# Kernel optimization log

Hardware: AMD Instinct MI355X
Metric: run time of the kernel (lower is better)

Reference implementation:

```python
import jax, jax.numpy as jnp
import numpy as np

B, S, D = 4, 2048, 512
K = 8192  # codebook_size
COMMIT_W = 0.25
ENT_W = 0.1
ENT_TEMP = 0.01
EPS = 1e-8


def setup_inputs() -> dict:
    key = jax.random.key(0)
    kx, kc = jax.random.split(key)
    x = jax.random.normal(kx, (B, S, D), dtype=jnp.float32)
    # variance_scaling(1.0, 'fan_in', 'uniform'): bound = sqrt(3 / fan_in)
    bound = np.sqrt(3.0 / D)
    codebook = jax.random.uniform(kc, (K, D), dtype=jnp.float32, minval=-bound, maxval=bound)
    return {"x": x, "codebook": codebook}


def _entropy_loss(affinity, temperature, eps=EPS):
    # affinity: (B, S, K) -> flatten tokens
    flat = affinity.reshape((-1, affinity.shape[-1])) / temperature
    probs = jax.nn.softmax(flat, axis=-1)
    log_probs = jax.nn.log_softmax(flat + eps, axis=-1)
    avg_probs = jnp.mean(probs, axis=0)
    avg_entropy = -jnp.sum(avg_probs * jnp.log(avg_probs + eps))
    sample_entropy = -jnp.mean(jnp.sum(probs * log_probs, axis=-1))
    return sample_entropy - avg_entropy


def reference(x, codebook):
    # the original cdist, without the (B,S,K,D) intermediate).
    x_sq = jnp.sum(x * x, axis=-1, keepdims=True)          # (B,S,1)
    c_sq = jnp.sum(codebook * codebook, axis=-1)           # (K,)
    dots = jnp.einsum('bsd,kd->bsk', x, codebook)          # (B,S,K)
    distances = jnp.sqrt(jnp.maximum(x_sq - 2.0 * dots + c_sq, 0.0))
    indices = jnp.argmin(distances, axis=-1)               # (B,S)
    # one_hot @ codebook == gather
    quantized = jnp.take(codebook, indices, axis=0)        # (B,S,D)

    sg = jax.lax.stop_gradient
    # optax.l2_loss(p, t) = 0.5 * (p - t)^2
    commit_loss = 0.5 * jnp.mean((x - sg(quantized)) ** 2) * COMMIT_W
    codebook_loss = 0.5 * jnp.mean((sg(x) - quantized) ** 2)
    entropy_loss = _entropy_loss(-distances, ENT_TEMP) * ENT_W
    loss = codebook_loss + commit_loss + entropy_loss

    quantized_st = x + sg(quantized - x)  # straight-through estimator
    return (quantized_st, loss, commit_loss, codebook_loss, entropy_loss, indices)
```

## Files before the change

### kernel.cpp

```cpp
#include <hip/hip_runtime.h>
#include <math.h>

#define NTOK 8192
#define KCODES 8192
#define DDIM 512
#define QELEMS (NTOK * DDIM)

#define NCHUNK 8
#define CPC (KCODES / NCHUNK)
#define LDK 40

constexpr size_t S_PART  = 0;
constexpr size_t S_XSQ   = 524288;
constexpr size_t S_CSQ   = S_XSQ + NTOK;
constexpr size_t S_LSE   = S_CSQ + KCODES;
constexpr size_t S_PLOGP = S_LSE + NTOK;
constexpr size_t S_D2    = S_PLOGP + NTOK;
constexpr size_t S_AVG   = S_D2 + NTOK;
constexpr size_t S_I1    = S_AVG + KCODES;
constexpr size_t S_I2    = S_I1 + NTOK;

#define NCHUNK_F 16
#define CPC_F (KCODES / NCHUNK_F)

constexpr size_t FS_PART  = 0;
constexpr size_t FS_XSQ   = 1048576;
constexpr size_t FS_CSQ   = FS_XSQ + NTOK;
constexpr size_t FS_LSE   = FS_CSQ + KCODES;
constexpr size_t FS_PLOGP = FS_LSE + NTOK;
constexpr size_t FS_D2    = FS_PLOGP + NTOK;
constexpr size_t FS_AVG   = FS_D2 + NTOK;
constexpr size_t FS_I1    = FS_AVG + KCODES;
constexpr size_t FS_I2    = FS_I1 + NTOK;

constexpr size_t WS_NEED_BYTES = 4ull * (size_t)QELEMS * 2ull;

typedef __attribute__((ext_vector_type(8))) short bf16x8;
typedef __attribute__((ext_vector_type(4))) float f32x4;

__device__ __forceinline__ bool better(float v, int i, float v2, int i2) {
  return v > v2 || (v == v2 && i < i2);
}

__device__ __forceinline__ void cvt_hilo(float f, unsigned& h, unsigned& l) {
  const unsigned u = __float_as_uint(f);
  h = u >> 16;
  const float lf = f - __uint_as_float(u & 0xFFFF0000u);
  l = __float_as_uint(lf) >> 16;
}

__device__ __forceinline__ void gll16(const unsigned short* g, const short* l) {
  __builtin_amdgcn_global_load_lds(
      (const __attribute__((address_space(1))) unsigned int*)g,
      (__attribute__((address_space(3))) unsigned int*)l, 16, 0, 0);
}

__global__ __launch_bounds__(64) void sq_kernel(const float* __restrict__ x,
                                                const float* __restrict__ cb,
                                                float* __restrict__ dout,
                                                size_t offXsq, size_t offCsq) {
  const int row = blockIdx.x;
  const int lane = threadIdx.x;
  const float* src = (row < KCODES) ? (cb + (size_t)row * DDIM)
                                    : (x + (size_t)(row - KCODES) * DDIM);
  float4 v0 = reinterpret_cast<const float4*>(src)[lane];
  float4 v1 = reinterpret_cast<const float4*>(src)[lane + 64];
  float s = v0.x*v0.x + v0.y*v0.y + v0.z*v0.z + v0.w*v0.w
          + v1.x*v1.x + v1.y*v1.y + v1.z*v1.z + v1.w*v1.w;
  #pragma unroll
  for (int o = 32; o; o >>= 1) s += __shfl_down(s, o);
  if (lane == 0) {
    if (row < KCODES) dout[offCsq + row] = s;
    else              dout[offXsq + (row - KCODES)] = s;
  }
}

__global__ void zero_kernel(float* __restrict__ dout, size_t offAvg) {
  dout[offAvg + blockIdx.x * 256 + threadIdx.x] = 0.f;
}

__global__ __launch_bounds__(256) void cvt_kernel(const float* __restrict__ x,
                                                  const float* __restrict__ cb,
                                                  unsigned short* __restrict__ ws) {
  const size_t fid = (size_t)blockIdx.x * 256 + threadIdx.x;
  const size_t half = (size_t)QELEMS / 4;
  const bool isX = fid < half;
  const float* src = isX ? x : cb;
  unsigned short* dh = ws + (isX ? 0 : (size_t)2 * QELEMS);
  unsigned short* dl = dh + QELEMS;
  const size_t f = isX ? fid : fid - half;
  const size_t e0 = f * 4;
  const int row = (int)(e0 >> 9);
  const int k = (int)(e0 & 511);
  const int tile = row >> 7, r = row & 127;
  const int kt = k >> 5, gg = (k >> 3) & 3, e = k & 7;
  const float4 v = *reinterpret_cast<const float4*>(src + e0);
  unsigned h0, h1, h2, h3, l0, l1, l2, l3;
  cvt_hilo(v.x, h0, l0); cvt_hilo(v.y, h1, l1);
  cvt_hilo(v.z, h2, l2); cvt_hilo(v.w, h3, l3);
  uint2 hp, lp;
  hp.x = h0 | (h1 << 16); hp.y = h2 | (h3 << 16);
  lp.x = l0 | (l1 << 16); lp.y = l2 | (l3 << 16);
  const size_t dst = (((size_t)tile * 16 + kt) * 4 + gg) * 1024 + (size_t)r * 8 + e;
  *reinterpret_cast<uint2*>(dh + dst) = hp;
  *reinterpret_cast<uint2*>(dl + dst) = lp;
}


#define MFMA_KSTEP_F                                                          \
  {                                                                           \
    bf16x8 a_h[4], a_l[4];                                                    \
    _Pragma("unroll")                                                         \
    for (int fi = 0; fi < 4; ++fi) {                                          \
      const int ra = (wr * 64 + fi * 16 + lx) * 8 + kg * 1024;                \
      a_h[fi] = *reinterpret_cast<const bf16x8*>(&lds4[0][ra]);               \
      a_l[fi] = *reinterpret_cast<const bf16x8*>(&lds4[1][ra]);               \
    }                                                                         \
    _Pragma("unroll")                                                         \
    for (int fj = 0; fj < 4; ++fj) {                                          \
      const int rb = (wc * 64 + fj * 16 + lx) * 8 + kg * 1024;                \
      const bf16x8 b_h = *reinterpret_cast<const bf16x8*>(&lds4[2][rb]);      \
      const bf16x8 b_l = *reinterpret_cast<const bf16x8*>(&lds4[3][rb]);      \
      _Pragma("unroll")                                                       \
      for (int fi = 0; fi < 4; ++fi) {                                        \
        acc[fi][fj] = __builtin_amdgcn_mfma_f32_16x16x32_bf16(a_h[fi], b_h, acc[fi][fj], 0, 0, 0); \
        acc[fi][fj] = __builtin_amdgcn_mfma_f32_16x16x32_bf16(a_l[fi], b_h, acc[fi][fj], 0, 0, 0); \
        acc[fi][fj] = __builtin_amdgcn_mfma_f32_16x16x32_bf16(a_h[fi], b_l, acc[fi][fj], 0, 0, 0); \
      }                                                                       \
    }                                                                         \
  }

#define STAGE_F(kt_)                                                          \
  {                                                                           \
    const unsigned short* p = gb + (((size_t)tile * 16 + (kt_)) * 4096) + l * 8; \
    const short* lb = &lds4[w][0];                                            \
    _Pragma("unroll")                                                         \
    for (int s8 = 0; s8 < 8; ++s8) gll16(p + s8 * 512, lb + s8 * 512);        \
  }

__global__ __launch_bounds__(256, 3) void pass1f(const unsigned short* __restrict__ ws,
                                                 float* __restrict__ dout) {
  __shared__ short lds4[4][4096];
  __shared__ float stats[2][128][6];
  const int tid = threadIdx.x;
  const int l = tid & 63;
  const int w = tid >> 6;
  const int wr = w >> 1, wc = w & 1;
  const int kg = l >> 4, lx = l & 15;
  const int m0 = blockIdx.y * 128;
  const int atile = blockIdx.y;
  const int chunk = blockIdx.x;

  if (tid < 128) {
    #pragma unroll
    for (int q = 0; q < 2; ++q) {
      stats[q][tid][0] = -1e30f; stats[q][tid][1] = 0.f; stats[q][tid][2] = 0.f;
      stats[q][tid][3] = -1e30f;
      stats[q][tid][4] = __int_as_float(0x7fffffff);
      stats[q][tid][5] = __int_as_float(0x7fffffff);
    }
  }

  float xs[16];
  #pragma unroll
  for (int fi = 0; fi < 4; ++fi)
    #pragma unroll
    for (int v = 0; v < 4; ++v)
      xs[fi * 4 + v] = dout[FS_XSQ + m0 + wr * 64 + fi * 16 + kg * 4 + v];

  const unsigned short* gb = ws + (size_t)w * (size_t)QELEMS;

  for (int st = 0; st < CPC_F / 128; ++st) {
    const int n0 = chunk * CPC_F + st * 128;
    const int tile = (w < 2) ? atile : (n0 >> 7);
    f32x4 acc[4][4];
    #pragma unroll
    for (int fi = 0; fi < 4; ++fi)
      #pragma unroll
      for (int fj = 0; fj < 4; ++fj)
        acc[fi][fj] = (f32x4){0.f, 0.f, 0.f, 0.f};

    for (int kt = 0; kt < DDIM / 32; ++kt) {
      __syncthreads();
      STAGE_F(kt);
      __syncthreads();
      MFMA_KSTEP_F;
    }

    const int colbase = n0 + wc * 64 + lx;
    float cs[4];
    #pragma unroll
    for (int fj = 0; fj < 4; ++fj) cs[fj] = dout[FS_CSQ + colbase + fj * 16];

    #pragma unroll
    for (int fi = 0; fi < 4; ++fi) {
      #pragma unroll
      for (int v = 0; v < 4; ++v) {
        const float xsv = xs[fi * 4 + v];
        float fv[4];
        #pragma unroll
        for (int fj = 0; fj < 4; ++fj) {
          const float d2 = fmaxf(fmaf(-2.f, acc[fi][fj][v], xsv) + cs[fj], 0.f);
          fv[fj] = -100.f * sqrtf(d2);
        }
        float v1 = fv[0], v2 = -1e30f;
        int i1 = colbase, i2 = 0x7fffffff;
        #pragma unroll
        for (int fj = 1; fj < 4; ++fj) {
          const int c = colbase + fj * 16;
          if (better(fv[fj], c, v1, i1)) { v2 = v1; i2 = i1; v1 = fv[fj]; i1 = c; }
          else if (better(fv[fj], c, v2, i2)) { v2 = fv[fj]; i2 = c; }
        }
        #pragma unroll
        for (int mask = 1; mask < 16; mask <<= 1) {
          const float ov1 = __shfl_xor(v1, mask);
          const float ov2 = __shfl_xor(v2, mask);
          const int oi1 = __shfl_xor(i1, mask);
          const int oi2 = __shfl_xor(i2, mask);
          float n1, n2; int ni1, ni2;
          if (better(ov1, oi1, v1, i1)) {
            n1 = ov1; ni1 = oi1;
            if (better(v1, i1, ov2, oi2)) { n2 = v1; ni2 = i1; } else { n2 = ov2; ni2 = oi2; }
          } else {
            n1 = v1; ni1 = i1;
            if (better(ov1, oi1, v2, i2)) { n2 = ov1; ni2 = oi1; } else { n2 = v2; ni2 = i2; }
          }
          v1 = n1; i1 = ni1; v2 = n2; i2 = ni2;
        }
        float z = 0.f, s = 0.f;
        #pragma unroll
        for (int fj = 0; fj < 4; ++fj) {
          const float ge = fv[fj] - v1;
          const float e = __expf(ge);
          z += e; s = fmaf(e, ge, s);
        }
        #pragma unroll
        for (int mask = 1; mask < 16; mask <<= 1) {
          z += __shfl_xor(z, mask);
          s += __shfl_xor(s, mask);
        }
        if (lx == 0) {
          const int r = wr * 64 + fi * 16 + kg * 4 + v;
          float* st_ = &stats[wc][r][0];
          const float ov1 = st_[0], oz = st_[1], os = st_[2], ov2 = st_[3];
          const int oi1 = __float_as_int(st_[4]), oi2 = __float_as_int(st_[5]);
          const float M = fmaxf(v1, ov1);
          const float ea = __expf(v1 - M), eb = __expf(ov1 - M);
          st_[1] = ea * z + eb * oz;
          st_[2] = ea * (s + (v1 - M) * z) + eb * (os + (ov1 - M) * oz);
          float n1, n2; int ni1, ni2;
          if (better(ov1, oi1, v1, i1)) {
            n1 = ov1; ni1 = oi1;
            if (better(v1, i1, ov2, oi2)) { n2 = v1; ni2 = i1; } else { n2 = ov2; ni2 = oi2; }
          } else {
            n1 = v1; ni1 = i1;
            if (better(ov1, oi1, v2, i2)) { n2 = ov1; ni2 = oi1; } else { n2 = v2; ni2 = i2; }
          }
          st_[0] = n1; st_[3] = n2;
          st_[4] = __int_as_float(ni1);
          st_[5] = __int_as_float(ni2);
        }
      }
    }
  }

  __syncthreads();
  if (tid < 128) {
    float v1 = stats[0][tid][0], z = stats[0][tid][1], s = stats[0][tid][2], v2 = stats[0][tid][3];
    int i1 = __float_as_int(stats[0][tid][4]), i2 = __float_as_int(stats[0][tid][5]);
    const float ov1 = stats[1][tid][0], oz = stats[1][tid][1];
    const float os = stats[1][tid][2], ov2 = stats[1][tid][3];
    const int oi1 = __float_as_int(stats[1][tid][4]), oi2 = __float_as_int(stats[1][tid][5]);
    const float M = fmaxf(v1, ov1);
    const float ea = __expf(v1 - M), eb = __expf(ov1 - M);
    const float nz = ea * z + eb * oz;
    const float ns = ea * (s + (v1 - M) * z) + eb * (os + (ov1 - M) * oz);
    float n1, n2; int ni1, ni2;
    if (better(ov1, oi1, v1, i1)) {
      n1 = ov1; ni1 = oi1;
      if (better(v1, i1, ov2, oi2)) { n2 = v1; ni2 = i1; } else { n2 = ov2; ni2 = oi2; }
    } else {
      n1 = v1; ni1 = i1;
      if (better(ov1, oi1, v2, i2)) { n2 = ov1; ni2 = oi1; } else { n2 = v2; ni2 = i2; }
    }
    float* p = dout + FS_PART + ((size_t)(m0 + tid) * NCHUNK_F + chunk) * 8;
    p[0] = n1; p[1] = nz; p[2] = ns; p[3] = n2;
    p[4] = __int_as_float(ni1); p[5] = __int_as_float(ni2);
  }
}

__global__ __launch_bounds__(256, 3) void colf(const unsigned short* __restrict__ ws,
                                               float* __restrict__ dout) {
  __shared__ short lds4[4][4096];
  __shared__ float red[4][64];
  const int tid = threadIdx.x;
  const int l = tid & 63;
  const int w = tid >> 6;
  const int wr = w >> 1, wc = w & 1;
  const int kg = l >> 4, lx = l & 15;
  const int m0 = blockIdx.y * 128;
  const int atile = blockIdx.y;
  const int chunk = blockIdx.x;

  float xs[16], lse[16];
  #pragma unroll
  for (int fi = 0; fi < 4; ++fi)
    #pragma unroll
    for (int v = 0; v < 4; ++v) {
      const int r = m0 + wr * 64 + fi * 16 + kg * 4 + v;
      xs[fi * 4 + v] = dout[FS_XSQ + r];
      lse[fi * 4 + v] = dout[FS_LSE + r];
    }

  const unsigned short* gb = ws + (size_t)w * (size_t)QELEMS;

  for (int st = 0; st < CPC_F / 128; ++st) {
    const int n0 = chunk * CPC_F + st * 128;
    const int tile = (w < 2) ? atile : (n0 >> 7);
    f32x4 acc[4][4];
    #pragma unroll
    for (int fi = 0; fi < 4; ++fi)
      #pragma unroll
      for (int fj = 0; fj < 4; ++fj)
        acc[fi][fj] = (f32x4){0.f, 0.f, 0.f, 0.f};

    for (int kt = 0; kt < DDIM / 32; ++kt) {
      __syncthreads();
      STAGE_F(kt);
      __syncthreads();
      MFMA_KSTEP_F;
    }

    const int colbase = n0 + wc * 64 + lx;
    float cs[4];
    #pragma unroll
    for (int fj = 0; fj < 4; ++fj) cs[fj] = dout[FS_CSQ + colbase + fj * 16];

    float colsum[4] = {0.f, 0.f, 0.f, 0.f};
    #pragma unroll
    for (int fi = 0; fi < 4; ++fi) {
      #pragma unroll
      for (int v = 0; v < 4; ++v) {
        const float xsv = xs[fi * 4 + v];
        const float lsev = lse[fi * 4 + v];
        #pragma unroll
        for (int fj = 0; fj < 4; ++fj) {
          const float d2 = fmaxf(fmaf(-2.f, acc[fi][fj][v], xsv) + cs[fj], 0.f);
          const float f = -100.f * sqrtf(d2);
          colsum[fj] += __expf(f - lsev);
        }
      }
    }
    #pragma unroll
    for (int fj = 0; fj < 4; ++fj) {
      colsum[fj] += __shfl_xor(colsum[fj], 16);
      colsum[fj] += __shfl_xor(colsum[fj], 32);
    }
    __syncthreads();
    if (kg == 0) {
      #pragma unroll
      for (int fj = 0; fj < 4; ++fj) red[w][fj * 16 + lx] = colsum[fj];
    }
    __syncthreads();
    if (tid < 128) {
      const int wcc = tid >> 6, c = tid & 63;
      atomicAdd(&dout[FS_AVG + n0 + tid], red[wcc][c] + red[wcc + 2][c]);
    }
  }
}


#define STAGE_TILES(kt_)                                                      \
  {                                                                           \
    const int kb = (kt_) * 32 + sc;                                           \
    _Pragma("unroll")                                                         \
    for (int rep = 0; rep < 4; ++rep) {                                       \
      const int row = sr + rep * 32;                                          \
      const float4 av = *reinterpret_cast<const float4*>(                     \
          x + (size_t)(m0 + row) * DDIM + kb);                                \
      const float4 bv = *reinterpret_cast<const float4*>(                     \
          cb + (size_t)(n0 + row) * DDIM + kb);                               \
      unsigned h0, h1, h2, h3, l0, l1, l2, l3;                                \
      uint2 t;                                                                \
      cvt_hilo(av.x, h0, l0); cvt_hilo(av.y, h1, l1);                         \
      cvt_hilo(av.z, h2, l2); cvt_hilo(av.w, h3, l3);                         \
      t.x = h0 | (h1 << 16); t.y = h2 | (h3 << 16);                           \
      *reinterpret_cast<uint2*>(&Ah[row][sc]) = t;                            \
      t.x = l0 | (l1 << 16); t.y = l2 | (l3 << 16);                           \
      *reinterpret_cast<uint2*>(&Al[row][sc]) = t;                            \
      cvt_hilo(bv.x, h0, l0); cvt_hilo(bv.y, h1, l1);                         \
      cvt_hilo(bv.z, h2, l2); cvt_hilo(bv.w, h3, l3);                         \
      t.x = h0 | (h1 << 16); t.y = h2 | (h3 << 16);                           \
      *reinterpret_cast<uint2*>(&Bh[row][sc]) = t;                            \
      t.x = l0 | (l1 << 16); t.y = l2 | (l3 << 16);                           \
      *reinterpret_cast<uint2*>(&Bl[row][sc]) = t;                            \
    }                                                                         \
  }

#define MFMA_KSTEP                                                            \
  {                                                                           \
    bf16x8 a_h[4], a_l[4];                                                    \
    _Pragma("unroll")                                                         \
    for (int fi = 0; fi < 4; ++fi) {                                          \
      a_h[fi] = *reinterpret_cast<const bf16x8*>(&Ah[ar + fi * 16][koff]);    \
      a_l[fi] = *reinterpret_cast<const bf16x8*>(&Al[ar + fi * 16][koff]);    \
    }                                                                         \
    _Pragma("unroll")                                                         \
    for (int fj = 0; fj < 4; ++fj) {                                          \
      const bf16x8 b_h = *reinterpret_cast<const bf16x8*>(&Bh[br + fj * 16][koff]); \
      const bf16x8 b_l = *reinterpret_cast<const bf16x8*>(&Bl[br + fj * 16][koff]); \
      _Pragma("unroll")                                                       \
      for (int fi = 0; fi < 4; ++fi) {                                        \
        acc[fi][fj] = __builtin_amdgcn_mfma_f32_16x16x32_bf16(a_h[fi], b_h, acc[fi][fj], 0, 0, 0); \
        acc[fi][fj] = __builtin_amdgcn_mfma_f32_16x16x32_bf16(a_l[fi], b_h, acc[fi][fj], 0, 0, 0); \
        acc[fi][fj] = __builtin_amdgcn_mfma_f32_16x16x32_bf16(a_h[fi], b_l, acc[fi][fj], 0, 0, 0); \
      }                                                                       \
    }                                                                         \
  }

__global__ __launch_bounds__(256) void pass1_mfma(const float* __restrict__ x,
                                                  const float* __restrict__ cb,
                                                  float* __restrict__ dout) {
  __shared__ short Ah[128][LDK], Al[128][LDK], Bh[128][LDK], Bl[128][LDK];
  __shared__ float stats[2][128][6];
  const int tid = threadIdx.x;
  const int l = tid & 63;
  const int w = tid >> 6;
  const int wr = w >> 1, wc = w & 1;
  const int g = l >> 4, lx = l & 15;
  const int ar = wr * 64 + lx;
  const int br = wc * 64 + lx;
  const int koff = g * 8;
  const int sr = tid >> 3;
  const int sc = (tid & 7) * 4;
  const int m0 = blockIdx.y * 128;
  const int chunk = blockIdx.x;

  if (tid < 128) {
    #pragma unroll
    for (int q = 0; q < 2; ++q) {
      stats[q][tid][0] = -1e30f; stats[q][tid][1] = 0.f; stats[q][tid][2] = 0.f;
      stats[q][tid][3] = -1e30f;
      stats[q][tid][4] = __int_as_float(0x7fffffff);
      stats[q][tid][5] = __int_as_float(0x7fffffff);
    }
  }

  float xs[16];
  #pragma unroll
  for (int fi = 0; fi < 4; ++fi)
    #pragma unroll
    for (int v = 0; v < 4; ++v)
      xs[fi * 4 + v] = dout[S_XSQ + m0 + wr * 64 + fi * 16 + g * 4 + v];

  for (int st = 0; st < CPC / 128; ++st) {
    const int n0 = chunk * CPC + st * 128;
    f32x4 acc[4][4];
    #pragma unroll
    for (int fi = 0; fi < 4; ++fi)
      #pragma unroll
      for (int fj = 0; fj < 4; ++fj)
        acc[fi][fj] = (f32x4){0.f, 0.f, 0.f, 0.f};

    for (int kt = 0; kt < DDIM / 32; ++kt) {
      __syncthreads();
      STAGE_TILES(kt);
      __syncthreads();
      MFMA_KSTEP;
    }

    const int colbase = n0 + wc * 64 + lx;
    float cs[4];
    #pragma unroll
    for (int fj = 0; fj < 4; ++fj) cs[fj] = dout[S_CSQ + colbase + fj * 16];

    #pragma unroll
    for (int fi = 0; fi < 4; ++fi) {
      #pragma unroll
      for (int v = 0; v < 4; ++v) {
        const float xsv = xs[fi * 4 + v];
        float fv[4];
        #pragma unroll
        for (int fj = 0; fj < 4; ++fj) {
          const float d2 = fmaxf(fmaf(-2.f, acc[fi][fj][v], xsv) + cs[fj], 0.f);
          fv[fj] = -100.f * sqrtf(d2);
        }
        float v1 = fv[0], v2 = -1e30f;
        int i1 = colbase, i2 = 0x7fffffff;
        #pragma unroll
        for (int fj = 1; fj < 4; ++fj) {
          const int c = colbase + fj * 16;
          if (better(fv[fj], c, v1, i1)) { v2 = v1; i2 = i1; v1 = fv[fj]; i1 = c; }
          else if (better(fv[fj], c, v2, i2)) { v2 = fv[fj]; i2 = c; }
        }
        #pragma unroll
        for (int mask = 1; mask < 16; mask <<= 1) {
          const float ov1 = __shfl_xor(v1, mask);
          const float ov2 = __shfl_xor(v2, mask);
          const int oi1 = __shfl_xor(i1, mask);
          const int oi2 = __shfl_xor(i2, mask);
          float n1, n2; int ni1, ni2;
          if (better(ov1, oi1, v1, i1)) {
            n1 = ov1; ni1 = oi1;
            if (better(v1, i1, ov2, oi2)) { n2 = v1; ni2 = i1; } else { n2 = ov2; ni2 = oi2; }
          } else {
            n1 = v1; ni1 = i1;
            if (better(ov1, oi1, v2, i2)) { n2 = ov1; ni2 = oi1; } else { n2 = v2; ni2 = i2; }
          }
          v1 = n1; i1 = ni1; v2 = n2; i2 = ni2;
        }
        float z = 0.f, s = 0.f;
        #pragma unroll
        for (int fj = 0; fj < 4; ++fj) {
          const float ge = fv[fj] - v1;
          const float e = __expf(ge);
          z += e; s = fmaf(e, ge, s);
        }
        #pragma unroll
        for (int mask = 1; mask < 16; mask <<= 1) {
          z += __shfl_xor(z, mask);
// ... 274 lines not shown
```

Before: 663.5 us.

## Double-buffer LDS staging and keep per-row online softmax stats in registers

Both the row-statistics and column-sum GEMM kernels now double-buffer their LDS tiles. The next k-slice is loaded asynchronously while MFMAs run on the current one, and each step needs one barrier instead of two. In pass1f the per-row argmin, top-2 and online softmax statistics are kept per lane in registers across all column tiles and reduced by shuffles only once at the end, instead of after every tile. In exchange, LDS use doubles and register pressure rises, so the occupancy hint is lowered from 3 to 2 blocks per CU.

```diff
diff --git a/kernel.cpp b/kernel.cpp
--- a/kernel.cpp
+++ b/kernel.cpp
@@ -107,20 +107,31 @@
 }
 
 
-#define MFMA_KSTEP_F                                                          \
+#define STAGE2(b_, s_)                                                        \
   {                                                                           \
+    const int st_ = (s_) >> 4, kt_ = (s_) & 15;                               \
+    const int tile_ = (w < 2) ? atile : ((chunk * CPC_F + st_ * 128) >> 7);   \
+    const unsigned short* p = gb + (((size_t)tile_ * 16 + kt_) * 4096) + l * 8; \
+    const short* lb = &lds4[b_][w][0];                                        \
+    _Pragma("unroll")                                                         \
+    for (int s8 = 0; s8 < 8; ++s8) gll16(p + s8 * 512, lb + s8 * 512);        \
+  }
+
+#define MFMA_KSTEP2(b_)                                                       \
+  {                                                                           \
+    const short* Lb = &lds4[b_][0][0];                                        \
     bf16x8 a_h[4], a_l[4];                                                    \
     _Pragma("unroll")                                                         \
     for (int fi = 0; fi < 4; ++fi) {                                          \
       const int ra = (wr * 64 + fi * 16 + lx) * 8 + kg * 1024;                \
-      a_h[fi] = *reinterpret_cast<const bf16x8*>(&lds4[0][ra]);               \
-      a_l[fi] = *reinterpret_cast<const bf16x8*>(&lds4[1][ra]);               \
+      a_h[fi] = *reinterpret_cast<const bf16x8*>(Lb + ra);                    \
+      a_l[fi] = *reinterpret_cast<const bf16x8*>(Lb + 4096 + ra);             \
     }                                                                         \
     _Pragma("unroll")                                                         \
     for (int fj = 0; fj < 4; ++fj) {                                          \
       const int rb = (wc * 64 + fj * 16 + lx) * 8 + kg * 1024;                \
-      const bf16x8 b_h = *reinterpret_cast<const bf16x8*>(&lds4[2][rb]);      \
-      const bf16x8 b_l = *reinterpret_cast<const bf16x8*>(&lds4[3][rb]);      \
+      const bf16x8 b_h = *reinterpret_cast<const bf16x8*>(Lb + 8192 + rb);    \
+      const bf16x8 b_l = *reinterpret_cast<const bf16x8*>(Lb + 12288 + rb);   \
       _Pragma("unroll")                                                       \
       for (int fi = 0; fi < 4; ++fi) {                                        \
         acc[fi][fj] = __builtin_amdgcn_mfma_f32_16x16x32_bf16(a_h[fi], b_h, acc[fi][fj], 0, 0, 0); \
@@ -130,17 +141,9 @@
     }                                                                         \
   }
 
-#define STAGE_F(kt_)                                                          \
-  {                                                                           \
-    const unsigned short* p = gb + (((size_t)tile * 16 + (kt_)) * 4096) + l * 8; \
-    const short* lb = &lds4[w][0];                                            \
-    _Pragma("unroll")                                                         \
-    for (int s8 = 0; s8 < 8; ++s8) gll16(p + s8 * 512, lb + s8 * 512);        \
-  }
-
-__global__ __launch_bounds__(256, 3) void pass1f(const unsigned short* __restrict__ ws,
+__global__ __launch_bounds__(256, 2) void pass1f(const unsigned short* __restrict__ ws,
                                                  float* __restrict__ dout) {
-  __shared__ short lds4[4][4096];
+  __shared__ short lds4[2][4][4096];
   __shared__ float stats[2][128][6];
   const int tid = threadIdx.x;
   const int l = tid & 63;
@@ -151,16 +154,6 @@
   const int atile = blockIdx.y;
   const int chunk = blockIdx.x;
 
-  if (tid < 128) {
-    #pragma unroll
-    for (int q = 0; q < 2; ++q) {
-      stats[q][tid][0] = -1e30f; stats[q][tid][1] = 0.f; stats[q][tid][2] = 0.f;
-      stats[q][tid][3] = -1e30f;
-      stats[q][tid][4] = __int_as_float(0x7fffffff);
-      stats[q][tid][5] = __int_as_float(0x7fffffff);
-    }
-  }
-
   float xs[16];
   #pragma unroll
   for (int fi = 0; fi < 4; ++fi)
@@ -168,99 +161,106 @@
     for (int v = 0; v < 4; ++v)
       xs[fi * 4 + v] = dout[FS_XSQ + m0 + wr * 64 + fi * 16 + kg * 4 + v];
 
+  float rv1[16], rv2[16], rz[16], rs[16];
+  int ri1[16], ri2[16];
+  #pragma unroll
+  for (int r = 0; r < 16; ++r) {
+    rv1[r] = -1e30f; rv2[r] = -1e30f; rz[r] = 0.f; rs[r] = 0.f;
+    ri1[r] = 0x7fffffff; ri2[r] = 0x7fffffff;
+  }
+
   const unsigned short* gb = ws + (size_t)w * (size_t)QELEMS;
 
-  for (int st = 0; st < CPC_F / 128; ++st) {
-    const int n0 = chunk * CPC_F + st * 128;
-    const int tile = (w < 2) ? atile : (n0 >> 7);
-    f32x4 acc[4][4];
-    #pragma unroll
-    for (int fi = 0; fi < 4; ++fi)
-      #pragma unroll
-      for (int fj = 0; fj < 4; ++fj)
-        acc[fi][fj] = (f32x4){0.f, 0.f, 0.f, 0.f};
-
-    for (int kt = 0; kt < DDIM / 32; ++kt) {
-      __syncthreads();
-      STAGE_F(kt);
-      __syncthreads();
-      MFMA_KSTEP_F;
-    }
-
-    const int colbase = n0 + wc * 64 + lx;
-    float cs[4];
-    #pragma unroll
-    for (int fj = 0; fj < 4; ++fj) cs[fj] = dout[FS_CSQ + colbase + fj * 16];
-
-    #pragma unroll
-    for (int fi = 0; fi < 4; ++fi) {
-      #pragma unroll
-      for (int v = 0; v < 4; ++v) {
-        const float xsv = xs[fi * 4 + v];
-        float fv[4];
-        #pragma unroll
-        for (int fj = 0; fj < 4; ++fj) {
-          const float d2 = fmaxf(fmaf(-2.f, acc[fi][fj][v], xsv) + cs[fj], 0.f);
-          fv[fj] = -100.f * sqrtf(d2);
-        }
-        float v1 = fv[0], v2 = -1e30f;
-        int i1 = colbase, i2 = 0x7fffffff;
-        #pragma unroll
-        for (int fj = 1; fj < 4; ++fj) {
-          const int c = colbase + fj * 16;
-          if (better(fv[fj], c, v1, i1)) { v2 = v1; i2 = i1; v1 = fv[fj]; i1 = c; }
-          else if (better(fv[fj], c, v2, i2)) { v2 = fv[fj]; i2 = c; }
-        }
-        #pragma unroll
-        for (int mask = 1; mask < 16; mask <<= 1) {
-          const float ov1 = __shfl_xor(v1, mask);
-          const float ov2 = __shfl_xor(v2, mask);
-          const int oi1 = __shfl_xor(i1, mask);
-          const int oi2 = __shfl_xor(i2, mask);
-          float n1, n2; int ni1, ni2;
-          if (better(ov1, oi1, v1, i1)) {
-            n1 = ov1; ni1 = oi1;
-            if (better(v1, i1, ov2, oi2)) { n2 = v1; ni2 = i1; } else { n2 = ov2; ni2 = oi2; }
-          } else {
-            n1 = v1; ni1 = i1;
-            if (better(ov1, oi1, v2, i2)) { n2 = ov1; ni2 = oi1; } else { n2 = v2; ni2 = i2; }
+  f32x4 acc[4][4];
+  #pragma unroll
+  for (int fi = 0; fi < 4; ++fi)
+    #pragma unroll
+    for (int fj = 0; fj < 4; ++fj)
+      acc[fi][fj] = (f32x4){0.f, 0.f, 0.f, 0.f};
+
+  STAGE2(0, 0);
+  __syncthreads();
+
+  for (int step = 0; step < 4 * 16; ++step) {
+    const int cur = step & 1;
+    if (step < 63) STAGE2(cur ^ 1, step + 1);
+    MFMA_KSTEP2(cur);
+
+    if ((step & 15) == 15) {
+      const int st = step >> 4;
+      const int n0 = chunk * CPC_F + st * 128;
+      const int colbase = n0 + wc * 64 + lx;
+      float cs[4];
+      #pragma unroll
+      for (int fj = 0; fj < 4; ++fj) cs[fj] = dout[FS_CSQ + colbase + fj * 16];
+
+      #pragma unroll
+      for (int fi = 0; fi < 4; ++fi) {
+        #pragma unroll
+        for (int v = 0; v < 4; ++v) {
+          const int r = fi * 4 + v;
+          const float xsv = xs[r];
+          #pragma unroll
+          for (int fj = 0; fj < 4; ++fj) {
+            const float d2 = fmaxf(fmaf(-2.f, acc[fi][fj][v], xsv) + cs[fj], 0.f);
+            const float f = -100.f * sqrtf(d2);
+            const int c = colbase + fj * 16;
+            if (f > rv1[r]) {
+              const float a = __expf(rv1[r] - f);
+              rs[r] = a * (rs[r] + (rv1[r] - f) * rz[r]);
+              rz[r] = fmaf(a, rz[r], 1.0f);
+              rv2[r] = rv1[r]; ri2[r] = ri1[r];
+              rv1[r] = f; ri1[r] = c;
+            } else {
+              const float g = f - rv1[r];
+              const float e = __expf(g);
+              rz[r] += e;
+              rs[r] = fmaf(e, g, rs[r]);
+              if (better(f, c, rv2[r], ri2[r])) { rv2[r] = f; ri2[r] = c; }
+            }
           }
-          v1 = n1; i1 = ni1; v2 = n2; i2 = ni2;
-        }
-        float z = 0.f, s = 0.f;
-        #pragma unroll
-        for (int fj = 0; fj < 4; ++fj) {
-          const float ge = fv[fj] - v1;
-          const float e = __expf(ge);
-          z += e; s = fmaf(e, ge, s);
-        }
-        #pragma unroll
-        for (int mask = 1; mask < 16; mask <<= 1) {
-          z += __shfl_xor(z, mask);
-          s += __shfl_xor(s, mask);
-        }
-        if (lx == 0) {
-          const int r = wr * 64 + fi * 16 + kg * 4 + v;
-          float* st_ = &stats[wc][r][0];
-          const float ov1 = st_[0], oz = st_[1], os = st_[2], ov2 = st_[3];
-          const int oi1 = __float_as_int(st_[4]), oi2 = __float_as_int(st_[5]);
-          const float M = fmaxf(v1, ov1);
-          const float ea = __expf(v1 - M), eb = __expf(ov1 - M);
-          st_[1] = ea * z + eb * oz;
-          st_[2] = ea * (s + (v1 - M) * z) + eb * (os + (ov1 - M) * oz);
-          float n1, n2; int ni1, ni2;
-          if (better(ov1, oi1, v1, i1)) {
-            n1 = ov1; ni1 = oi1;
-            if (better(v1, i1, ov2, oi2)) { n2 = v1; ni2 = i1; } else { n2 = ov2; ni2 = oi2; }
-          } else {
-            n1 = v1; ni1 = i1;
-            if (better(ov1, oi1, v2, i2)) { n2 = ov1; ni2 = oi1; } else { n2 = v2; ni2 = i2; }
-          }
-          st_[0] = n1; st_[3] = n2;
-          st_[4] = __int_as_float(ni1);
-          st_[5] = __int_as_float(ni2);
         }
       }
+      #pragma unroll
+      for (int fi = 0; fi < 4; ++fi)
+        #pragma unroll
+        for (int fj = 0; fj < 4; ++fj)
+          acc[fi][fj] = (f32x4){0.f, 0.f, 0.f, 0.f};
+    }
+    __syncthreads();
+  }
+
+  #pragma unroll
+  for (int r = 0; r < 16; ++r) {
+    float v1 = rv1[r], v2 = rv2[r], z = rz[r], s = rs[r];
+    int i1 = ri1[r], i2 = ri2[r];
+    #pragma unroll
+    for (int mask = 1; mask < 16; mask <<= 1) {
+      const float ov1 = __shfl_xor(v1, mask);
+      const float ov2 = __shfl_xor(v2, mask);
+      const float oz  = __shfl_xor(z, mask);
+      const float os  = __shfl_xor(s, mask);
+      const int oi1 = __shfl_xor(i1, mask);
+      const int oi2 = __shfl_xor(i2, mask);
+      const float M = fmaxf(v1, ov1);
+      const float ea = __expf(v1 - M), eb = __expf(ov1 - M);
+      s = ea * (s + (v1 - M) * z) + eb * (os + (ov1 - M) * oz);
+      z = ea * z + eb * oz;
+      float n1, n2; int ni1, ni2;
+      if (better(ov1, oi1, v1, i1)) {
+        n1 = ov1; ni1 = oi1;
+        if (better(v1, i1, ov2, oi2)) { n2 = v1; ni2 = i1; } else { n2 = ov2; ni2 = oi2; }
+      } else {
+        n1 = v1; ni1 = i1;
+        if (better(ov1, oi1, v2, i2)) { n2 = ov1; ni2 = oi1; } else { n2 = v2; ni2 = i2; }
+      }
+      v1 = n1; i1 = ni1; v2 = n2; i2 = ni2;
+    }
+    if (lx == 0) {
+      const int row = wr * 64 + (r >> 2) * 16 + kg * 4 + (r & 3);
+      float* st_ = &stats[wc][row][0];
+      st_[0] = v1; st_[1] = z; st_[2] = s; st_[3] = v2;
+      st_[4] = __int_as_float(i1); st_[5] = __int_as_float(i2);
     }
   }
 
@@ -289,9 +289,9 @@
   }
 }
 
-__global__ __launch_bounds__(256, 3) void colf(const unsigned short* __restrict__ ws,
+__global__ __launch_bounds__(256, 2) void colf(const unsigned short* __restrict__ ws,
                                                float* __restrict__ dout) {
-  __shared__ short lds4[4][4096];
+  __shared__ short lds4[2][4][4096];
   __shared__ float red[4][64];
   const int tid = threadIdx.x;
   const int l = tid & 63;
@@ -314,58 +314,66 @@
 
   const unsigned short* gb = ws + (size_t)w * (size_t)QELEMS;
 
-  for (int st = 0; st < CPC_F / 128; ++st) {
-    const int n0 = chunk * CPC_F + st * 128;
-    const int tile = (w < 2) ? atile : (n0 >> 7);
-    f32x4 acc[4][4];
-    #pragma unroll
-    for (int fi = 0; fi < 4; ++fi)
-      #pragma unroll
-      for (int fj = 0; fj < 4; ++fj)
-        acc[fi][fj] = (f32x4){0.f, 0.f, 0.f, 0.f};
-
-    for (int kt = 0; kt < DDIM / 32; ++kt) {
-      __syncthreads();
-      STAGE_F(kt);
-      __syncthreads();
-      MFMA_KSTEP_F;
-    }
-
-    const int colbase = n0 + wc * 64 + lx;
-    float cs[4];
-    #pragma unroll
-    for (int fj = 0; fj < 4; ++fj) cs[fj] = dout[FS_CSQ + colbase + fj * 16];
-
-    float colsum[4] = {0.f, 0.f, 0.f, 0.f};
-    #pragma unroll
-    for (int fi = 0; fi < 4; ++fi) {
-      #pragma unroll
-      for (int v = 0; v < 4; ++v) {
-        const float xsv = xs[fi * 4 + v];
-        const float lsev = lse[fi * 4 + v];
-        #pragma unroll
-        for (int fj = 0; fj < 4; ++fj) {
-          const float d2 = fmaxf(fmaf(-2.f, acc[fi][fj][v], xsv) + cs[fj], 0.f);
-          const float f = -100.f * sqrtf(d2);
-          colsum[fj] += __expf(f - lsev);
+  f32x4 acc[4][4];
+  #pragma unroll
+  for (int fi = 0; fi < 4; ++fi)
+    #pragma unroll
+    for (int fj = 0; fj < 4; ++fj)
+      acc[fi][fj] = (f32x4){0.f, 0.f, 0.f, 0.f};
+
+  STAGE2(0, 0);
+  __syncthreads();
+
+  for (int step = 0; step < 4 * 16; ++step) {
+    const int cur = step & 1;
+    if (step < 63) STAGE2(cur ^ 1, step + 1);
+    MFMA_KSTEP2(cur);
+
+    if ((step & 15) == 15) {
+      const int st = step >> 4;
+      const int n0 = chunk * CPC_F + st * 128;
+      const int colbase = n0 + wc * 64 + lx;
+      float cs[4];
+      #pragma unroll
+      for (int fj = 0; fj < 4; ++fj) cs[fj] = dout[FS_CSQ + colbase + fj * 16];
+
+      float colsum[4] = {0.f, 0.f, 0.f, 0.f};
+      #pragma unroll
+      for (int fi = 0; fi < 4; ++fi) {
+        #pragma unroll
+        for (int v = 0; v < 4; ++v) {
+          const float xsv = xs[fi * 4 + v];
+          const float lsev = lse[fi * 4 + v];
+          #pragma unroll
+          for (int fj = 0; fj < 4; ++fj) {
+            const float d2 = fmaxf(fmaf(-2.f, acc[fi][fj][v], xsv) + cs[fj], 0.f);
+            const float f = -100.f * sqrtf(d2);
+            colsum[fj] += __expf(f - lsev);
+          }
         }
       }
-    }
-    #pragma unroll
-    for (int fj = 0; fj < 4; ++fj) {
-      colsum[fj] += __shfl_xor(colsum[fj], 16);
-      colsum[fj] += __shfl_xor(colsum[fj], 32);
+      #pragma unroll
+      for (int fj = 0; fj < 4; ++fj) {
+        colsum[fj] += __shfl_xor(colsum[fj], 16);
+        colsum[fj] += __shfl_xor(colsum[fj], 32);
+      }
+      __syncthreads();
+      if (kg == 0) {
+        #pragma unroll
+        for (int fj = 0; fj < 4; ++fj) red[w][fj * 16 + lx] = colsum[fj];
+      }
+      __syncthreads();
+      if (tid < 128) {
+        const int wcc = tid >> 6, c = tid & 63;
+        atomicAdd(&dout[FS_AVG + n0 + tid], red[wcc][c] + red[wcc + 2][c]);
+      }
+      #pragma unroll
+      for (int fi = 0; fi < 4; ++fi)
+        #pragma unroll
+        for (int fj = 0; fj < 4; ++fj)
+          acc[fi][fj] = (f32x4){0.f, 0.f, 0.f, 0.f};
     }
     __syncthreads();
-    if (kg == 0) {
-      #pragma unroll
-      for (int fj = 0; fj < 4; ++fj) red[w][fj * 16 + lx] = colsum[fj];
-    }
-    __syncthreads();
-    if (tid < 128) {
-      const int wcc = tid >> 6, c = tid & 63;
-      atomicAdd(&dout[FS_AVG + n0 + tid], red[wcc][c] + red[wcc + 2][c]);
-    }
   }
 }
 
```

Measured after the change: 725.5 us. 1.09x slower.

## Double-buffer LDS staging in pass1f and colf, drop lo-part MFMAs in colf

Applied to the files above, without the earlier changes.

Flattens the codebook-strip and k-step loops of pass1f and colf into one software-pipelined loop. Two LDS buffers alternate, so the global-to-LDS copy of the next k-step overlaps the MFMAs on the current one. The per-strip epilogue now runs once every 16 steps. colf also stops using the bf16 hi/lo split: it stages and multiplies only the hi halves, which cuts its MFMA count and staging traffic but lowers the precision of the column-sum probabilities. Launch bounds change to 2 blocks per CU for pass1f, which doubles its LDS use, and to 4 for colf.

```diff
diff --git a/kernel.cpp b/kernel.cpp
--- a/kernel.cpp
+++ b/kernel.cpp
@@ -107,20 +107,30 @@
 }
 
 
-#define MFMA_KSTEP_F                                                          \
+#define STAGE_P1(dst_, s_)                                                    \
+  {                                                                           \
+    const int st_ = (s_) >> 4, kt_ = (s_) & 15;                               \
+    const int tile_ = (w < 2) ? atile : ((chunk * CPC_F + st_ * 128) >> 7);   \
+    const unsigned short* p = gb + (((size_t)tile_ * 16 + kt_) * 4096) + l * 8; \
+    const short* lb = &dst_[w][0];                                            \
+    _Pragma("unroll")                                                         \
+    for (int s8 = 0; s8 < 8; ++s8) gll16(p + s8 * 512, lb + s8 * 512);        \
+  }
+
+#define MFMA_P1(src_)                                                         \
   {                                                                           \
     bf16x8 a_h[4], a_l[4];                                                    \
     _Pragma("unroll")                                                         \
     for (int fi = 0; fi < 4; ++fi) {                                          \
       const int ra = (wr * 64 + fi * 16 + lx) * 8 + kg * 1024;                \
-      a_h[fi] = *reinterpret_cast<const bf16x8*>(&lds4[0][ra]);               \
-      a_l[fi] = *reinterpret_cast<const bf16x8*>(&lds4[1][ra]);               \
+      a_h[fi] = *reinterpret_cast<const bf16x8*>(&src_[0][ra]);               \
+      a_l[fi] = *reinterpret_cast<const bf16x8*>(&src_[1][ra]);               \
     }                                                                         \
     _Pragma("unroll")                                                         \
     for (int fj = 0; fj < 4; ++fj) {                                          \
       const int rb = (wc * 64 + fj * 16 + lx) * 8 + kg * 1024;                \
-      const bf16x8 b_h = *reinterpret_cast<const bf16x8*>(&lds4[2][rb]);      \
-      const bf16x8 b_l = *reinterpret_cast<const bf16x8*>(&lds4[3][rb]);      \
+      const bf16x8 b_h = *reinterpret_cast<const bf16x8*>(&src_[2][rb]);      \
+      const bf16x8 b_l = *reinterpret_cast<const bf16x8*>(&src_[3][rb]);      \
       _Pragma("unroll")                                                       \
       for (int fi = 0; fi < 4; ++fi) {                                        \
         acc[fi][fj] = __builtin_amdgcn_mfma_f32_16x16x32_bf16(a_h[fi], b_h, acc[fi][fj], 0, 0, 0); \
@@ -130,17 +140,94 @@
     }                                                                         \
   }
 
-#define STAGE_F(kt_)                                                          \
+#define EPI_P1(st_)                                                           \
   {                                                                           \
-    const unsigned short* p = gb + (((size_t)tile * 16 + (kt_)) * 4096) + l * 8; \
-    const short* lb = &lds4[w][0];                                            \
-    _Pragma("unroll")                                                         \
-    for (int s8 = 0; s8 < 8; ++s8) gll16(p + s8 * 512, lb + s8 * 512);        \
-  }
-
-__global__ __launch_bounds__(256, 3) void pass1f(const unsigned short* __restrict__ ws,
+    const int n0 = chunk * CPC_F + (st_) * 128;                               \
+    const int colbase = n0 + wc * 64 + lx;                                    \
+    float cs[4];                                                              \
+    _Pragma("unroll")                                                         \
+    for (int fj = 0; fj < 4; ++fj) cs[fj] = dout[FS_CSQ + colbase + fj * 16]; \
+    _Pragma("unroll")                                                         \
+    for (int fi = 0; fi < 4; ++fi) {                                          \
+      _Pragma("unroll")                                                       \
+      for (int v = 0; v < 4; ++v) {                                           \
+        const float xsv = xs[fi * 4 + v];                                     \
+        float fv[4];                                                          \
+        _Pragma("unroll")                                                     \
+        for (int fj = 0; fj < 4; ++fj) {                                      \
+          const float d2 = fmaxf(fmaf(-2.f, acc[fi][fj][v], xsv) + cs[fj], 0.f); \
+          fv[fj] = -100.f * sqrtf(d2);                                        \
+        }                                                                     \
+        float v1 = fv[0], v2 = -1e30f;                                        \
+        int i1 = colbase, i2 = 0x7fffffff;                                    \
+        _Pragma("unroll")                                                     \
+        for (int fj = 1; fj < 4; ++fj) {                                      \
+          const int c = colbase + fj * 16;                                    \
+          if (better(fv[fj], c, v1, i1)) { v2 = v1; i2 = i1; v1 = fv[fj]; i1 = c; } \
+          else if (better(fv[fj], c, v2, i2)) { v2 = fv[fj]; i2 = c; }        \
+        }                                                                     \
+        _Pragma("unroll")                                                     \
+        for (int mask = 1; mask < 16; mask <<= 1) {                           \
+          const float ov1 = __shfl_xor(v1, mask);                             \
+          const float ov2 = __shfl_xor(v2, mask);                             \
+          const int oi1 = __shfl_xor(i1, mask);                               \
+          const int oi2 = __shfl_xor(i2, mask);                               \
+          float n1, n2; int ni1, ni2;                                         \
+          if (better(ov1, oi1, v1, i1)) {                                     \
+            n1 = ov1; ni1 = oi1;                                              \
+            if (better(v1, i1, ov2, oi2)) { n2 = v1; ni2 = i1; } else { n2 = ov2; ni2 = oi2; } \
+          } else {                                                            \
+            n1 = v1; ni1 = i1;                                                \
+            if (better(ov1, oi1, v2, i2)) { n2 = ov1; ni2 = oi1; } else { n2 = v2; ni2 = i2; } \
+          }                                                                   \
+          v1 = n1; i1 = ni1; v2 = n2; i2 = ni2;                               \
+        }                                                                     \
+        float z = 0.f, s = 0.f;                                               \
+        _Pragma("unroll")                                                     \
+        for (int fj = 0; fj < 4; ++fj) {                                      \
+          const float ge = fv[fj] - v1;                                       \
+          const float e = __expf(ge);                                         \
+          z += e; s = fmaf(e, ge, s);                                         \
+        }                                                                     \
+        _Pragma("unroll")                                                     \
+        for (int mask = 1; mask < 16; mask <<= 1) {                           \
+          z += __shfl_xor(z, mask);                                           \
+          s += __shfl_xor(s, mask);                                           \
+        }                                                                     \
+        if (lx == 0) {                                                        \
+          const int r = wr * 64 + fi * 16 + kg * 4 + v;                       \
+          float* st2 = &stats[wc][r][0];                                      \
+          const float ov1 = st2[0], oz = st2[1], os = st2[2], ov2 = st2[3];   \
+          const int oi1 = __float_as_int(st2[4]), oi2 = __float_as_int(st2[5]); \
+          const float M = fmaxf(v1, ov1);                                     \
+          const float ea = __expf(v1 - M), eb = __expf(ov1 - M);              \
+          st2[1] = ea * z + eb * oz;                                          \
+          st2[2] = ea * (s + (v1 - M) * z) + eb * (os + (ov1 - M) * oz);      \
+          float n1, n2; int ni1, ni2;                                         \
+          if (better(ov1, oi1, v1, i1)) {                                     \
+            n1 = ov1; ni1 = oi1;                                              \
+            if (better(v1, i1, ov2, oi2)) { n2 = v1; ni2 = i1; } else { n2 = ov2; ni2 = oi2; } \
+          } else {                                                            \
+            n1 = v1; ni1 = i1;                                                \
+            if (better(ov1, oi1, v2, i2)) { n2 = ov1; ni2 = oi1; } else { n2 = v2; ni2 = i2; } \
+          }                                                                   \
+          st2[0] = n1; st2[3] = n2;                                           \
+          st2[4] = __int_as_float(ni1);                                       \
+          st2[5] = __int_as_float(ni2);                                       \
+        }                                                                     \
+      }                                                                       \
+    }                                                                         \
+    _Pragma("unroll")                                                         \
+    for (int fi = 0; fi < 4; ++fi)                                            \
+      _Pragma("unroll")                                                       \
+      for (int fj = 0; fj < 4; ++fj)                                          \
+        acc[fi][fj] = (f32x4){0.f, 0.f, 0.f, 0.f};                            \
+  }
+
+__global__ __launch_bounds__(256, 2) void pass1f(const unsigned short* __restrict__ ws,
                                                  float* __restrict__ dout) {
-  __shared__ short lds4[4][4096];
+  __shared__ short ldsA[4][4096];
+  __shared__ short ldsB[4][4096];
   __shared__ float stats[2][128][6];
   const int tid = threadIdx.x;
   const int l = tid & 63;
@@ -170,101 +257,27 @@
 
   const unsigned short* gb = ws + (size_t)w * (size_t)QELEMS;
 
-  for (int st = 0; st < CPC_F / 128; ++st) {
-    const int n0 = chunk * CPC_F + st * 128;
-    const int tile = (w < 2) ? atile : (n0 >> 7);
-    f32x4 acc[4][4];
-    #pragma unroll
-    for (int fi = 0; fi < 4; ++fi)
-      #pragma unroll
-      for (int fj = 0; fj < 4; ++fj)
-        acc[fi][fj] = (f32x4){0.f, 0.f, 0.f, 0.f};
-
-    for (int kt = 0; kt < DDIM / 32; ++kt) {
-      __syncthreads();
-      STAGE_F(kt);
-      __syncthreads();
-      MFMA_KSTEP_F;
-    }
-
-    const int colbase = n0 + wc * 64 + lx;
-    float cs[4];
-    #pragma unroll
-    for (int fj = 0; fj < 4; ++fj) cs[fj] = dout[FS_CSQ + colbase + fj * 16];
-
-    #pragma unroll
-    for (int fi = 0; fi < 4; ++fi) {
-      #pragma unroll
-      for (int v = 0; v < 4; ++v) {
-        const float xsv = xs[fi * 4 + v];
-        float fv[4];
-        #pragma unroll
-        for (int fj = 0; fj < 4; ++fj) {
-          const float d2 = fmaxf(fmaf(-2.f, acc[fi][fj][v], xsv) + cs[fj], 0.f);
-          fv[fj] = -100.f * sqrtf(d2);
-        }
-        float v1 = fv[0], v2 = -1e30f;
-        int i1 = colbase, i2 = 0x7fffffff;
-        #pragma unroll
-        for (int fj = 1; fj < 4; ++fj) {
-          const int c = colbase + fj * 16;
-          if (better(fv[fj], c, v1, i1)) { v2 = v1; i2 = i1; v1 = fv[fj]; i1 = c; }
-          else if (better(fv[fj], c, v2, i2)) { v2 = fv[fj]; i2 = c; }
-        }
-        #pragma unroll
-        for (int mask = 1; mask < 16; mask <<= 1) {
-          const float ov1 = __shfl_xor(v1, mask);
-          const float ov2 = __shfl_xor(v2, mask);
-          const int oi1 = __shfl_xor(i1, mask);
-          const int oi2 = __shfl_xor(i2, mask);
-          float n1, n2; int ni1, ni2;
-          if (better(ov1, oi1, v1, i1)) {
-            n1 = ov1; ni1 = oi1;
-            if (better(v1, i1, ov2, oi2)) { n2 = v1; ni2 = i1; } else { n2 = ov2; ni2 = oi2; }
-          } else {
-            n1 = v1; ni1 = i1;
-            if (better(ov1, oi1, v2, i2)) { n2 = ov1; ni2 = oi1; } else { n2 = v2; ni2 = i2; }
-          }
-          v1 = n1; i1 = ni1; v2 = n2; i2 = ni2;
-        }
-        float z = 0.f, s = 0.f;
-        #pragma unroll
-        for (int fj = 0; fj < 4; ++fj) {
-          const float ge = fv[fj] - v1;
-          const float e = __expf(ge);
-          z += e; s = fmaf(e, ge, s);
-        }
-        #pragma unroll
-        for (int mask = 1; mask < 16; mask <<= 1) {
-          z += __shfl_xor(z, mask);
-          s += __shfl_xor(s, mask);
-        }
-        if (lx == 0) {
-          const int r = wr * 64 + fi * 16 + kg * 4 + v;
-          float* st_ = &stats[wc][r][0];
-          const float ov1 = st_[0], oz = st_[1], os = st_[2], ov2 = st_[3];
-          const int oi1 = __float_as_int(st_[4]), oi2 = __float_as_int(st_[5]);
-          const float M = fmaxf(v1, ov1);
-          const float ea = __expf(v1 - M), eb = __expf(ov1 - M);
-          st_[1] = ea * z + eb * oz;
-          st_[2] = ea * (s + (v1 - M) * z) + eb * (os + (ov1 - M) * oz);
-          float n1, n2; int ni1, ni2;
-          if (better(ov1, oi1, v1, i1)) {
-            n1 = ov1; ni1 = oi1;
-            if (better(v1, i1, ov2, oi2)) { n2 = v1; ni2 = i1; } else { n2 = ov2; ni2 = oi2; }
-          } else {
-            n1 = v1; ni1 = i1;
-            if (better(ov1, oi1, v2, i2)) { n2 = ov1; ni2 = oi1; } else { n2 = v2; ni2 = i2; }
-          }
-          st_[0] = n1; st_[3] = n2;
-          st_[4] = __int_as_float(ni1);
-          st_[5] = __int_as_float(ni2);
-        }
-      }
-    }
-  }
-
+  f32x4 acc[4][4];
+  #pragma unroll
+  for (int fi = 0; fi < 4; ++fi)
+    #pragma unroll
+    for (int fj = 0; fj < 4; ++fj)
+      acc[fi][fj] = (f32x4){0.f, 0.f, 0.f, 0.f};
+
+  STAGE_P1(ldsA, 0);
   __syncthreads();
+
+  for (int i = 0; i < 32; ++i) {
+    const int so = 2 * i + 1;
+    STAGE_P1(ldsB, so);
+    MFMA_P1(ldsA);
+    __syncthreads();
+    if (so < 63) STAGE_P1(ldsA, so + 1);
+    MFMA_P1(ldsB);
+    if ((so & 15) == 15) EPI_P1(so >> 4);
+    __syncthreads();
+  }
+
   if (tid < 128) {
     float v1 = stats[0][tid][0], z = stats[0][tid][1], s = stats[0][tid][2], v2 = stats[0][tid][3];
     int i1 = __float_as_int(stats[0][tid][4]), i2 = __float_as_int(stats[0][tid][5]);
@@ -289,9 +302,84 @@
   }
 }
 
-__global__ __launch_bounds__(256, 3) void colf(const unsigned short* __restrict__ ws,
+#define STAGE_CF(dst_, s_)                                                    \
+  {                                                                           \
+    const int st_ = (s_) >> 4, kt_ = (s_) & 15;                               \
+    const int tile_ = (w < 2) ? atile : ((chunk * CPC_F + st_ * 128) >> 7);   \
+    const unsigned short* base = ws + ((w < 2) ? (size_t)0 : (size_t)2 * QELEMS); \
+    const unsigned short* p = base + (((size_t)tile_ * 16 + kt_) * 4096)      \
+                              + (size_t)(w & 1) * 2048 + l * 8;               \
+    const short* lb = &dst_[w >> 1][(w & 1) * 2048];                          \
+    _Pragma("unroll")                                                         \
+    for (int s8 = 0; s8 < 4; ++s8) gll16(p + s8 * 512, lb + s8 * 512);        \
+  }
+
+#define MFMA_CF(src_)                                                         \
+  {                                                                           \
+    bf16x8 a_h[4];                                                            \
+    _Pragma("unroll")                                                         \
+    for (int fi = 0; fi < 4; ++fi) {                                          \
+      const int ra = (wr * 64 + fi * 16 + lx) * 8 + kg * 1024;                \
+      a_h[fi] = *reinterpret_cast<const bf16x8*>(&src_[0][ra]);               \
+    }                                                                         \
+    _Pragma("unroll")                                                         \
+    for (int fj = 0; fj < 4; ++fj) {                                          \
+      const int rb = (wc * 64 + fj * 16 + lx) * 8 + kg * 1024;                \
+      const bf16x8 b_h = *reinterpret_cast<const bf16x8*>(&src_[1][rb]);      \
+      _Pragma("unroll")                                                       \
+      for (int fi = 0; fi < 4; ++fi)                                          \
+        acc[fi][fj] = __builtin_amdgcn_mfma_f32_16x16x32_bf16(a_h[fi], b_h, acc[fi][fj], 0, 0, 0); \
+    }                                                                         \
+  }
+
+#define EPI_CF(st_)                                                           \
+  {                                                                           \
+    const int n0 = chunk * CPC_F + (st_) * 128;                               \
+    const int colbase = n0 + wc * 64 + lx;                                    \
+    float cs[4];                                                              \
+    _Pragma("unroll")                                                         \
+    for (int fj = 0; fj < 4; ++fj) cs[fj] = dout[FS_CSQ + colbase + fj * 16]; \
+    float colsum[4] = {0.f, 0.f, 0.f, 0.f};                                   \
+    _Pragma("unroll")                                                         \
+    for (int fi = 0; fi < 4; ++fi) {                                          \
+      _Pragma("unroll")                                                       \
+      for (int v = 0; v < 4; ++v) {                                           \
+        const float xsv = xs[fi * 4 + v];                                     \
+        const float lsev = lse[fi * 4 + v];                                   \
+        _Pragma("unroll")                                                     \
+        for (int fj = 0; fj < 4; ++fj) {                                      \
+          const float d2 = fmaxf(fmaf(-2.f, acc[fi][fj][v], xsv) + cs[fj], 0.f); \
+          const float f = -100.f * sqrtf(d2);                                 \
+          colsum[fj] += __expf(f - lsev);                                     \
+        }                                                                     \
+      }                                                                       \
+    }                                                                         \
+    _Pragma("unroll")                                                         \
+    for (int fj = 0; fj < 4; ++fj) {                                          \
+      colsum[fj] += __shfl_xor(colsum[fj], 16);                               \
+      colsum[fj] += __shfl_xor(colsum[fj], 32);                               \
+    }                                                                         \
+    __syncthreads();                                                          \
+    if (kg == 0) {                                                            \
+      _Pragma("unroll")                                                       \
+      for (int fj = 0; fj < 4; ++fj) red[w][fj * 16 + lx] = colsum[fj];       \
+    }                                                                         \
+    __syncthreads();                                                          \
+    if (tid < 128) {                                                          \
+      const int wcc = tid >> 6, c = tid & 63;                                 \
+      atomicAdd(&dout[FS_AVG + n0 + tid], red[wcc][c] + red[wcc + 2][c]);     \
+    }                                                                         \
+    _Pragma("unroll")                                                         \
+    for (int fi = 0; fi < 4; ++fi)                                            \
+      _Pragma("unroll")                                                       \
+      for (int fj = 0; fj < 4; ++fj)                                          \
+        acc[fi][fj] = (f32x4){0.f, 0.f, 0.f, 0.f};                            \
+  }
+
+__global__ __launch_bounds__(256, 4) void colf(const unsigned short* __restrict__ ws,
                                                float* __restrict__ dout) {
-  __shared__ short lds4[4][4096];
+  __shared__ short ldsHA[2][4096];
+  __shared__ short ldsHB[2][4096];
   __shared__ float red[4][64];
   const int tid = threadIdx.x;
   const int l = tid & 63;
@@ -312,60 +400,25 @@
       lse[fi * 4 + v] = dout[FS_LSE + r];
     }
 
-  const unsigned short* gb = ws + (size_t)w * (size_t)QELEMS;
-
-  for (int st = 0; st < CPC_F / 128; ++st) {
-    const int n0 = chunk * CPC_F + st * 128;
-    const int tile = (w < 2) ? atile : (n0 >> 7);
-    f32x4 acc[4][4];
-    #pragma unroll
-    for (int fi = 0; fi < 4; ++fi)
-      #pragma unroll
-      for (int fj = 0; fj < 4; ++fj)
-        acc[fi][fj] = (f32x4){0.f, 0.f, 0.f, 0.f};
-
-    for (int kt = 0; kt < DDIM / 32; ++kt) {
-      __syncthreads();
-      STAGE_F(kt);
-      __syncthreads();
-      MFMA_KSTEP_F;
-    }
-
-    const int colbase = n0 + wc * 64 + lx;
-    float cs[4];
-    #pragma unroll
-    for (int fj = 0; fj < 4; ++fj) cs[fj] = dout[FS_CSQ + colbase + fj * 16];
-
-    float colsum[4] = {0.f, 0.f, 0.f, 0.f};
-    #pragma unroll
-    for (int fi = 0; fi < 4; ++fi) {
-      #pragma unroll
-      for (int v = 0; v < 4; ++v) {
-        const float xsv = xs[fi * 4 + v];
-        const float lsev = lse[fi * 4 + v];
-        #pragma unroll
-        for (int fj = 0; fj < 4; ++fj) {
-          const float d2 = fmaxf(fmaf(-2.f, acc[fi][fj][v], xsv) + cs[fj], 0.f);
-          const float f = -100.f * sqrtf(d2);
-          colsum[fj] += __expf(f - lsev);
-        }
-      }
-    }
-    #pragma unroll
-    for (int fj = 0; fj < 4; ++fj) {
-      colsum[fj] += __shfl_xor(colsum[fj], 16);
-      colsum[fj] += __shfl_xor(colsum[fj], 32);
-    }
+  f32x4 acc[4][4];
+  #pragma unroll
+  for (int fi = 0; fi < 4; ++fi)
+    #pragma unroll
+    for (int fj = 0; fj < 4; ++fj)
+      acc[fi][fj] = (f32x4){0.f, 0.f, 0.f, 0.f};
+
+  STAGE_CF(ldsHA, 0);
+  __syncthreads();
+
+  for (int i = 0; i < 32; ++i) {
+    const int so = 2 * i + 1;
+    STAGE_CF(ldsHB, so);
+    MFMA_CF(ldsHA);
     __syncthreads();
-    if (kg == 0) {
-      #pragma unroll
-      for (int fj = 0; fj < 4; ++fj) red[w][fj * 16 + lx] = colsum[fj];
-    }
+    if (so < 63) STAGE_CF(ldsHA, so + 1);
+    MFMA_CF(ldsHB);
+    if ((so & 15) == 15) EPI_CF(so >> 4);
     __syncthreads();
-    if (tid < 128) {
-      const int wcc = tid >> 6, c = tid & 63;
-      atomicAdd(&dout[FS_AVG + n0 + tid], red[wcc][c] + red[wcc + 2][c]);
-    }
   }
 }
 
```

After: 576.2 us. -13.2%, faster.
